# Kernel tuning notes

Hardware: AMD Instinct MI355X
Metric: run time of the kernel (lower is better)

## Reference

```python
import jax, jax.numpy as jnp
import numpy as np

SIZE = 1024
N_ITER = 10
TEMP = 0.125


def setup_inputs() -> dict:
    key = jax.random.key(0)
    k1, k2 = jax.random.split(key)
    x = jax.random.normal(k1, (8, 4096, SIZE), dtype=jnp.float32)
    # weight init: identity + small gaussian noise (matches torch init)
    weight = jnp.eye(SIZE, dtype=jnp.float32) + jax.random.normal(k2, (SIZE, SIZE), dtype=jnp.float32) * 1e-05
    return {"x": x, "weight": weight}


def _sinkhorn_project(weight):
    # log-space Sinkhorn normalization: n_iter steps of symmetric row/col
    # logsumexp subtraction, then exponentiate.
    log_P = weight / TEMP
    for _ in range(N_ITER):
        r_sum = jax.nn.logsumexp(log_P, axis=-1, keepdims=True)  # [size,1]
        c_sum = jax.nn.logsumexp(log_P, axis=-2, keepdims=True)  # [1,size]
        log_P = log_P - 0.5 * (r_sum + c_sum)
    return jnp.exp(log_P)


def reference(x, weight):
    W = _sinkhorn_project(weight)          # [size, size]
    # F.linear(x, W) == x @ W.T
    return jnp.einsum('bsd,od->bso', x, W)
```

## Files before the change

### kernel.cpp

```cpp
#include <hip/hip_runtime.h>
#include <hip/hip_bf16.h>


typedef __attribute__((ext_vector_type(8))) short short8;
typedef __attribute__((ext_vector_type(4))) float f32x4;

__device__ inline unsigned int pk2(float a, float b) {
  __hip_bfloat162 h = __float22bfloat162_rn(make_float2(a, b));
  union { __hip_bfloat162 h; unsigned int u; } cv;
  cv.h = h;
  return cv.u;
}

__global__ void sinkhorn_step(const float* __restrict__ w,
                              const float* __restrict__ Rin,
                              const float* __restrict__ Cin,
                              float* __restrict__ Rout,
                              float* __restrict__ Cout,
                              int first,
                              const float* __restrict__ X,
                              unsigned short* __restrict__ Xb,
                              int do_cvt) {
  __shared__ float4 red4[256];
  const int tid = threadIdx.x;
  const int b = blockIdx.x;
  const int lane = tid & 63, wv = tid >> 6;
  if (b < 256) {
    const int row = 4 * b + wv;
    const float* rp = w + (size_t)row * 1024 + lane * 16;
    float s = 0.f;
    #pragma unroll
    for (int q = 0; q < 4; ++q) {
      float4 v4 = *(const float4*)(rp + q * 4);
      float4 c4 = make_float4(0.f, 0.f, 0.f, 0.f);
      if (!first) c4 = *(const float4*)(Cin + lane * 16 + q * 4);
      s += __expf(8.f * v4.x - 0.5f * c4.x) + __expf(8.f * v4.y - 0.5f * c4.y)
         + __expf(8.f * v4.z - 0.5f * c4.z) + __expf(8.f * v4.w - 0.5f * c4.w);
    }
    #pragma unroll
    for (int off = 32; off > 0; off >>= 1) s += __shfl_down(s, off);
    if (lane == 0)
      Rout[row] = (first ? 0.f : 0.5f * Rin[row]) + __logf(s);
  } else if (b < 320) {
    const int cb = b - 256;
    const int c0 = cb * 16;
    const int rowg = tid >> 2, cg = tid & 3;
    const float* wp = w + (size_t)rowg * 1024 + c0 + cg * 4;
    float ax = 0.f, ay = 0.f, az = 0.f, aw = 0.f;
    #pragma unroll 4
    for (int p = 0; p < 16; ++p) {
      float4 wv4 = *(const float4*)(wp + (size_t)p * 64 * 1024);
      float rp = first ? 0.f : Rin[rowg + p * 64];
      float h = 0.5f * rp;
      ax += __expf(8.f * wv4.x - h);
      ay += __expf(8.f * wv4.y - h);
      az += __expf(8.f * wv4.z - h);
      aw += __expf(8.f * wv4.w - h);
    }
    red4[tid] = make_float4(ax, ay, az, aw);
    __syncthreads();
    if (tid < 16) {
      const int g = tid >> 2, e = tid & 3;
      float s = 0.f;
      #pragma unroll 8
      for (int q = 0; q < 64; ++q)
        s += ((const float*)&red4[q * 4 + g])[e];
      const int col = c0 + tid;
      Cout[col] = (first ? 0.f : 0.5f * Cin[col]) + __logf(s);
    }
  } else if (do_cvt) {
    const size_t idx0 = (size_t)(b - 320) * 256 + tid;
    #pragma unroll
    for (int it = 0; it < 8; ++it) {
      size_t e = (it * 524288ull + idx0) * 8;
      float4 a = *(const float4*)(X + e);
      float4 c = *(const float4*)(X + e + 4);
      uint4 o;
      o.x = pk2(a.x, a.y); o.y = pk2(a.z, a.w);
      o.z = pk2(c.x, c.y); o.w = pk2(c.z, c.w);
      *(uint4*)(Xb + e) = o;
    }
  }
}

__global__ void make_w(const float* __restrict__ w, const float* __restrict__ R,
                       const float* __restrict__ C, unsigned short* __restrict__ Wb) {
  const int i = blockIdx.x;
  const int j = threadIdx.x * 4;
  const float r = 0.5f * R[i];
  float4 v = *(const float4*)(w + (size_t)i * 1024 + j);
  float4 cv = *(const float4*)(C + j);
  unsigned int o[2];
  o[0] = pk2(__expf(8.f * v.x - r - 0.5f * cv.x), __expf(8.f * v.y - r - 0.5f * cv.y));
  o[1] = pk2(__expf(8.f * v.z - r - 0.5f * cv.z), __expf(8.f * v.w - r - 0.5f * cv.w));
  *(uint2*)(Wb + (size_t)i * 1024 + j) = *(uint2*)o;
}

__device__ inline void swizzle_mn(int id, int& m0, int& n0) {
  m0 = ((id & 7) + ((id >> 6) << 3)) << 7;
  n0 = ((id >> 3) & 7) << 7;
}

__global__ __launch_bounds__(256) void gemm_bb(const unsigned short* __restrict__ Xb,
                                               const unsigned short* __restrict__ Wb,
                                               float* __restrict__ out) {
  __shared__ unsigned short As[128 * 64];
  __shared__ unsigned short Bs[128 * 64];
  const int tid = threadIdx.x;
  const int lane = tid & 63, wave = tid >> 6;
  const int wm = wave >> 1, wn = wave & 1;
  int m0, n0;
  swizzle_mn(blockIdx.x, m0, n0);

  f32x4 acc[4][4] = {};
  const int fr = lane & 15, kq = lane >> 4;

  for (int t = 0; t < 16; ++t) {
    const int k0 = t * 64;
    #pragma unroll
    for (int is = 0; is < 4; ++is) {
      int idx = is * 256 + tid;
      int lrow = idx >> 3;
      int g = (idx & 7) ^ (lrow & 7);
      const unsigned short* ga = Xb + (size_t)(m0 + lrow) * 1024 + k0 + g * 8;
      const unsigned short* gb = Wb + (size_t)(n0 + lrow) * 1024 + k0 + g * 8;
      unsigned short* la = As + (size_t)(is * 256 + wave * 64) * 8;
      unsigned short* lb = Bs + (size_t)(is * 256 + wave * 64) * 8;
      __builtin_amdgcn_global_load_lds(
          (const __attribute__((address_space(1))) unsigned int*)ga,
          (__attribute__((address_space(3))) unsigned int*)la, 16, 0, 0);
      __builtin_amdgcn_global_load_lds(
          (const __attribute__((address_space(1))) unsigned int*)gb,
          (__attribute__((address_space(3))) unsigned int*)lb, 16, 0, 0);
    }
    __syncthreads();

    #pragma unroll
    for (int kk = 0; kk < 2; ++kk) {
      short8 af[4], bf[4];
      #pragma unroll
      for (int mt = 0; mt < 4; ++mt) {
        int row = wm * 64 + mt * 16 + fr;
        int cp = (kk * 4 + kq) ^ (row & 7);
        af[mt] = *(const short8*)(As + (size_t)row * 64 + cp * 8);
      }
      #pragma unroll
      for (int nt = 0; nt < 4; ++nt) {
        int row = wn * 64 + nt * 16 + fr;
        int cp = (kk * 4 + kq) ^ (row & 7);
        bf[nt] = *(const short8*)(Bs + (size_t)row * 64 + cp * 8);
      }
      #pragma unroll
      for (int mt = 0; mt < 4; ++mt)
        #pragma unroll
        for (int nt = 0; nt < 4; ++nt)
          acc[mt][nt] = __builtin_amdgcn_mfma_f32_16x16x32_bf16(af[mt], bf[nt], acc[mt][nt], 0, 0, 0);
    }
    __syncthreads();
  }

  const int crow0 = m0 + wm * 64 + (lane >> 4) * 4;
  const int ccol0 = n0 + wn * 64 + fr;
  #pragma unroll
  for (int mt = 0; mt < 4; ++mt)
    #pragma unroll
    for (int nt = 0; nt < 4; ++nt)
      #pragma unroll
      for (int r = 0; r < 4; ++r)
        out[(size_t)(crow0 + mt * 16 + r) * 1024 + ccol0 + nt * 16] = acc[mt][nt][r];
}

__global__ __launch_bounds__(256) void gemm_f(const float* __restrict__ X,
                                              const unsigned short* __restrict__ Wb,
                                              float* __restrict__ out) {
  __shared__ unsigned short As[128 * 64];
  __shared__ unsigned short Bs[128 * 64];
  const int tid = threadIdx.x;
  const int lane = tid & 63, wave = tid >> 6;
  const int wm = wave >> 1, wn = wave & 1;
  int m0, n0;
  swizzle_mn(blockIdx.x, m0, n0);

  f32x4 acc[4][4] = {};
  const int ar = tid >> 1, ah = tid & 1;
  const float* Xrow = X + (size_t)(m0 + ar) * 1024 + ah * 32;
  const int fr = lane & 15, kq = lane >> 4;

  for (int t = 0; t < 16; ++t) {
    const int k0 = t * 64;
    #pragma unroll
    for (int is = 0; is < 4; ++is) {
      int idx = is * 256 + tid;
      int lrow = idx >> 3;
      int g = (idx & 7) ^ (lrow & 7);
      const unsigned short* gb = Wb + (size_t)(n0 + lrow) * 1024 + k0 + g * 8;
      unsigned short* lb = Bs + (size_t)(is * 256 + wave * 64) * 8;
      __builtin_amdgcn_global_load_lds(
          (const __attribute__((address_space(1))) unsigned int*)gb,
          (__attribute__((address_space(3))) unsigned int*)lb, 16, 0, 0);
    }
    #pragma unroll
    for (int q = 0; q < 4; ++q) {
      float4 a = *(const float4*)(Xrow + k0 + q * 8);
      float4 c = *(const float4*)(Xrow + k0 + q * 8 + 4);
      uint4 o;
      o.x = pk2(a.x, a.y); o.y = pk2(a.z, a.w);
      o.z = pk2(c.x, c.y); o.w = pk2(c.z, c.w);
      int cp = (ah * 4 + q) ^ (ar & 7);
      *(uint4*)(As + (size_t)ar * 64 + cp * 8) = o;
    }
    __syncthreads();

    #pragma unroll
    for (int kk = 0; kk < 2; ++kk) {
      short8 af[4], bf[4];
      #pragma unroll
      for (int mt = 0; mt < 4; ++mt) {
        int row = wm * 64 + mt * 16 + fr;
        int cp = (kk * 4 + kq) ^ (row & 7);
        af[mt] = *(const short8*)(As + (size_t)row * 64 + cp * 8);
      }
      #pragma unroll
      for (int nt = 0; nt < 4; ++nt) {
        int row = wn * 64 + nt * 16 + fr;
        int cp = (kk * 4 + kq) ^ (row & 7);
        bf[nt] = *(const short8*)(Bs + (size_t)row * 64 + cp * 8);
      }
      #pragma unroll
      for (int mt = 0; mt < 4; ++mt)
        #pragma unroll
        for (int nt = 0; nt < 4; ++nt)
          acc[mt][nt] = __builtin_amdgcn_mfma_f32_16x16x32_bf16(af[mt], bf[nt], acc[mt][nt], 0, 0, 0);
    }
    __syncthreads();
  }

  const int crow0 = m0 + wm * 64 + (lane >> 4) * 4;
  const int ccol0 = n0 + wn * 64 + fr;
  #pragma unroll
  for (int mt = 0; mt < 4; ++mt)
    #pragma unroll
    for (int nt = 0; nt < 4; ++nt)
      #pragma unroll
      for (int r = 0; r < 4; ++r)
        out[(size_t)(crow0 + mt * 16 + r) * 1024 + ccol0 + nt * 16] = acc[mt][nt][r];
}

__global__ __launch_bounds__(256) void gemm_b(const float* __restrict__ X,
                                              const float* __restrict__ w,
                                              const float* __restrict__ R,
                                              const float* __restrict__ C,
                                              float* __restrict__ out) {
  __shared__ unsigned short As[128 * 32];
  __shared__ unsigned short Bs[128 * 32];
  const int tid = threadIdx.x;
  const int lane = tid & 63, wave = tid >> 6;
  const int wm = wave >> 1, wn = wave & 1;
  int m0, n0;
  swizzle_mn(blockIdx.x, m0, n0);

  f32x4 acc[4][4] = {};
  const int sr = tid >> 1, sk = (tid & 1) * 16;
  const float* Xrow = X + (size_t)(m0 + sr) * 1024 + sk;
  const float* Wrow = w + (size_t)(n0 + sr) * 1024 + sk;
  const float rpot = 0.5f * R[n0 + sr];

  for (int k0 = 0; k0 < 1024; k0 += 32) {
    float4 vb0 = *(const float4*)(Wrow + k0);
    float4 vb1 = *(const float4*)(Wrow + k0 + 4);
    float4 vb2 = *(const float4*)(Wrow + k0 + 8);
    float4 vb3 = *(const float4*)(Wrow + k0 + 12);
    float4 vc0 = *(const float4*)(C + k0 + sk);
    float4 vc1 = *(const float4*)(C + k0 + sk + 4);
    float4 vc2 = *(const float4*)(C + k0 + sk + 8);
    float4 vc3 = *(const float4*)(C + k0 + sk + 12);
    unsigned int pb[8];
    pb[0] = pk2(__expf(8.f * vb0.x - rpot - 0.5f * vc0.x), __expf(8.f * vb0.y - rpot - 0.5f * vc0.y));
    pb[1] = pk2(__expf(8.f * vb0.z - rpot - 0.5f * vc0.z), __expf(8.f * vb0.w - rpot - 0.5f * vc0.w));
    pb[2] = pk2(__expf(8.f * vb1.x - rpot - 0.5f * vc1.x), __expf(8.f * vb1.y - rpot - 0.5f * vc1.y));
    pb[3] = pk2(__expf(8.f * vb1.z - rpot - 0.5f * vc1.z), __expf(8.f * vb1.w - rpot - 0.5f * vc1.w));
    pb[4] = pk2(__expf(8.f * vb2.x - rpot - 0.5f * vc2.x), __expf(8.f * vb2.y - rpot - 0.5f * vc2.y));
    pb[5] = pk2(__expf(8.f * vb2.z - rpot - 0.5f * vc2.z), __expf(8.f * vb2.w - rpot - 0.5f * vc2.w));
    pb[6] = pk2(__expf(8.f * vb3.x - rpot - 0.5f * vc3.x), __expf(8.f * vb3.y - rpot - 0.5f * vc3.y));
    pb[7] = pk2(__expf(8.f * vb3.z - rpot - 0.5f * vc3.z), __expf(8.f * vb3.w - rpot - 0.5f * vc3.w));
    float4 va0 = *(const float4*)(Xrow + k0);
    float4 va1 = *(const float4*)(Xrow + k0 + 4);
    float4 va2 = *(const float4*)(Xrow + k0 + 8);
    float4 va3 = *(const float4*)(Xrow + k0 + 12);
    unsigned int pa[8];
    pa[0] = pk2(va0.x, va0.y); pa[1] = pk2(va0.z, va0.w);
    pa[2] = pk2(va1.x, va1.y); pa[3] = pk2(va1.z, va1.w);
    pa[4] = pk2(va2.x, va2.y); pa[5] = pk2(va2.z, va2.w);
    pa[6] = pk2(va3.x, va3.y); pa[7] = pk2(va3.z, va3.w);

    *(uint4*)(Bs + sr * 32 + sk)     = *(uint4*)(pb);
    *(uint4*)(Bs + sr * 32 + sk + 8) = *(uint4*)(pb + 4);
    *(uint4*)(As + sr * 32 + sk)     = *(uint4*)(pa);
    *(uint4*)(As + sr * 32 + sk + 8) = *(uint4*)(pa + 4);

    __syncthreads();

    const int kq2 = (lane >> 4) * 8;
    const int fr2 = lane & 15;
    short8 af[4], bf[4];
    #pragma unroll
    for (int t = 0; t < 4; ++t)
      af[t] = *(const short8*)(As + (wm * 64 + t * 16 + fr2) * 32 + kq2);
    #pragma unroll
    for (int t = 0; t < 4; ++t)
      bf[t] = *(const short8*)(Bs + (wn * 64 + t * 16 + fr2) * 32 + kq2);
    #pragma unroll
    for (int mt = 0; mt < 4; ++mt)
      #pragma unroll
      for (int nt = 0; nt < 4; ++nt)
        acc[mt][nt] = __builtin_amdgcn_mfma_f32_16x16x32_bf16(af[mt], bf[nt], acc[mt][nt], 0, 0, 0);

    __syncthreads();
  }

  const int crow0 = m0 + wm * 64 + (lane >> 4) * 4;
  const int ccol0 = n0 + wn * 64 + (lane & 15);
  #pragma unroll
  for (int mt = 0; mt < 4; ++mt)
    #pragma unroll
    for (int nt = 0; nt < 4; ++nt)
      #pragma unroll
      for (int r = 0; r < 4; ++r)
        out[(size_t)(crow0 + mt * 16 + r) * 1024 + ccol0 + nt * 16] = acc[mt][nt][r];
}

extern "C" void kernel_launch(void* const* d_in, const int* in_sizes, int n_in,
                              void* d_out, int out_size, void* d_ws, size_t ws_size,
                              hipStream_t stream) {
  const float* x = (const float*)d_in[0];
  const float* weight = (const float*)d_in[1];
  float* out = (float*)d_out;

  float* R0 = (float*)d_ws;
  float* C0 = R0 + 1024;
  float* R1 = C0 + 1024;
  float* C1 = R1 + 1024;
  unsigned short* Wb = (unsigned short*)(C1 + 1024);
  unsigned short* Xb = Wb + (size_t)1024 * 1024;
  const size_t need_small = 16 * 1024 + 2 * 1024 * 1024;
  const size_t need_big = need_small + (size_t)32768 * 1024 * 2;
  const int big = (ws_size >= need_big) ? 1 : 0;
  const int small_ok = (ws_size >= need_small) ? 1 : 0;

  for (int t = 0; t < 10; ++t) {
    const float *Ri, *Ci;
    float *Ro, *Co;
    if ((t & 1) == 0) { Ri = R0; Ci = C0; Ro = R1; Co = C1; }
    else              { Ri = R1; Ci = C1; Ro = R0; Co = C0; }
    const int cvt = (t == 0 && big) ? 1 : 0;
    const int grid = cvt ? 2368 : 320;
    sinkhorn_step<<<grid, 256, 0, stream>>>(weight, Ri, Ci, Ro, Co,
                                            (t == 0) ? 1 : 0, x, Xb, cvt);
  }

  if (small_ok) {
    make_w<<<1024, 256, 0, stream>>>(weight, R0, C0, Wb);
    if (big) gemm_bb<<<2048, 256, 0, stream>>>(Xb, Wb, out);
    else     gemm_f<<<2048, 256, 0, stream>>>(x, Wb, out);
  } else {
    gemm_b<<<2048, 256, 0, stream>>>(x, weight, R0, C0, out);
  }
}
```

Measured before the change: 377.5 us.

## Fuse Sinkhorn iterations into one persistent cooperative kernel with grid barriers

Replaces the ten separate sinkhorn_step launches and the make_w launch with a single cooperative persistent kernel of 256 blocks. Each block keeps its exp(weight/T) row and column slices in registers and runs the iterations in scaling-vector (u,v) form. The blocks synchronise through an atomic counter barrier in workspace, and the x-to-bf16 conversion is spread across the iterations between barrier arrive and wait. This removes per-launch overhead and the repeated weight reads. In exchange it relies on all blocks being co-resident, and a spin limit that can break out before every block arrives, which would give wrong results.

```diff
diff --git a/kernel.cpp b/kernel.cpp
--- a/kernel.cpp
+++ b/kernel.cpp
@@ -10,6 +10,172 @@
   union { __hip_bfloat162 h; unsigned int u; } cv;
   cv.h = h;
   return cv.u;
+}
+
+__device__ __forceinline__ void stc(float* p, float v) {
+  __hip_atomic_store(p, v, __ATOMIC_RELAXED, __HIP_MEMORY_SCOPE_AGENT);
+}
+__device__ __forceinline__ float ldc(const float* p) {
+  return __hip_atomic_load(p, __ATOMIC_RELAXED, __HIP_MEMORY_SCOPE_AGENT);
+}
+
+__global__ __launch_bounds__(256, 1) void sinkhorn_persist(
+    const float* __restrict__ w,
+    int* __restrict__ bar,
+    float* __restrict__ ubuf,
+    float* __restrict__ vbuf,
+    unsigned short* __restrict__ Wb,
+    const float* __restrict__ X,
+    unsigned short* __restrict__ Xb) {
+  __shared__ float uL[1024];
+  __shared__ float vL[1024];
+  __shared__ float redC[4][4];
+  const int k = blockIdx.x;
+  const int t = threadIdx.x;
+  const int l = t & 63, wv = t >> 6;
+  const int row = 4 * k + wv;
+
+  float er[16];
+  {
+    const float* rp = w + (size_t)row * 1024 + l * 16;
+    #pragma unroll
+    for (int q = 0; q < 4; ++q) {
+      float4 v4 = *(const float4*)(rp + q * 4);
+      er[q * 4 + 0] = __expf(8.f * v4.x);
+      er[q * 4 + 1] = __expf(8.f * v4.y);
+      er[q * 4 + 2] = __expf(8.f * v4.z);
+      er[q * 4 + 3] = __expf(8.f * v4.w);
+    }
+  }
+  float ecs[4][4];
+  {
+    #pragma unroll
+    for (int q = 0; q < 4; ++q) {
+      float4 v4 = *(const float4*)(w + (size_t)(4 * t + q) * 1024 + 4 * k);
+      ecs[q][0] = __expf(8.f * v4.x);
+      ecs[q][1] = __expf(8.f * v4.y);
+      ecs[q][2] = __expf(8.f * v4.z);
+      ecs[q][3] = __expf(8.f * v4.w);
+    }
+  }
+
+  float vold = 1.f;
+  float uold = 1.f;
+
+  for (int it = 0; it < 10; ++it) {
+    const int rsl = it & 1;
+    const int wsl = (it + 1) & 1;
+    float ul[16], vvr[4];
+    if (it == 0) {
+      #pragma unroll
+      for (int q = 0; q < 16; ++q) ul[q] = 1.f;
+      vvr[0] = vvr[1] = vvr[2] = vvr[3] = 1.f;
+    } else {
+      {
+        float u0 = ldc(ubuf + rsl * 1024 + t * 4);
+        float u1 = ldc(ubuf + rsl * 1024 + t * 4 + 1);
+        float u2 = ldc(ubuf + rsl * 1024 + t * 4 + 2);
+        float u3 = ldc(ubuf + rsl * 1024 + t * 4 + 3);
+        float v0 = ldc(vbuf + rsl * 1024 + t * 4);
+        float v1 = ldc(vbuf + rsl * 1024 + t * 4 + 1);
+        float v2 = ldc(vbuf + rsl * 1024 + t * 4 + 2);
+        float v3 = ldc(vbuf + rsl * 1024 + t * 4 + 3);
+        int cp = t ^ ((t >> 3) & 7);
+        *(float4*)(uL + cp * 4) = make_float4(u0, u1, u2, u3);
+        *(float4*)(vL + t * 4) = make_float4(v0, v1, v2, v3);
+      }
+      __syncthreads();
+      #pragma unroll
+      for (int q = 0; q < 4; ++q) {
+        int c = l * 4 + q;
+        int cp = c ^ ((c >> 3) & 7);
+        float4 u4 = *(const float4*)(uL + cp * 4);
+        ul[q * 4 + 0] = u4.x; ul[q * 4 + 1] = u4.y;
+        ul[q * 4 + 2] = u4.z; ul[q * 4 + 3] = u4.w;
+      }
+      float4 v4 = *(const float4*)(vL + t * 4);
+      vvr[0] = v4.x; vvr[1] = v4.y; vvr[2] = v4.z; vvr[3] = v4.w;
+    }
+
+    float rs = 0.f;
+    #pragma unroll
+    for (int q = 0; q < 16; ++q) rs += er[q] * ul[q];
+    #pragma unroll
+    for (int off = 32; off > 0; off >>= 1) rs += __shfl_down(rs, off);
+
+    float cs0 = 0.f, cs1 = 0.f, cs2 = 0.f, cs3 = 0.f;
+    #pragma unroll
+    for (int q = 0; q < 4; ++q) {
+      cs0 += ecs[q][0] * vvr[q]; cs1 += ecs[q][1] * vvr[q];
+      cs2 += ecs[q][2] * vvr[q]; cs3 += ecs[q][3] * vvr[q];
+    }
+    #pragma unroll
+    for (int off = 32; off > 0; off >>= 1) {
+      cs0 += __shfl_down(cs0, off); cs1 += __shfl_down(cs1, off);
+      cs2 += __shfl_down(cs2, off); cs3 += __shfl_down(cs3, off);
+    }
+    if (l == 0) {
+      redC[wv][0] = cs0; redC[wv][1] = cs1;
+      redC[wv][2] = cs2; redC[wv][3] = cs3;
+      vold = sqrtf(vold) * rsqrtf(rs);
+      stc(vbuf + wsl * 1024 + row, vold);
+    }
+    __syncthreads();
+    if (wv == 0 && l < 4) {
+      float tot = redC[0][l] + redC[1][l] + redC[2][l] + redC[3][l];
+      uold = sqrtf(uold) * rsqrtf(tot);
+      stc(ubuf + wsl * 1024 + 4 * k + l, uold);
+    }
+
+    asm volatile("s_waitcnt vmcnt(0)" ::: "memory");
+    __syncthreads();
+    if (t == 0)
+      __hip_atomic_fetch_add(bar + it, 1, __ATOMIC_RELAXED, __HIP_MEMORY_SCOPE_AGENT);
+    if (it < 8) {
+      const size_t base = (size_t)k * 131072 + (size_t)it * 16384;
+      #pragma unroll
+      for (int r2 = 0; r2 < 8; ++r2) {
+        size_t e = base + (size_t)(r2 * 256 + t) * 8;
+        float4 a = *(const float4*)(X + e);
+        float4 c = *(const float4*)(X + e + 4);
+        uint4 o;
+        o.x = pk2(a.x, a.y); o.y = pk2(a.z, a.w);
+        o.z = pk2(c.x, c.y); o.w = pk2(c.z, c.w);
+        *(uint4*)(Xb + e) = o;
+      }
+    }
+    if (t == 0) {
+      int spins = 0;
+      while (__hip_atomic_load(bar + it, __ATOMIC_RELAXED, __HIP_MEMORY_SCOPE_AGENT) < 256) {
+        __builtin_amdgcn_s_sleep(2);
+        if (++spins > (1 << 16)) break;
+      }
+    }
+    __syncthreads();
+  }
+
+  {
+    float u0 = ldc(ubuf + t * 4);
+    float u1 = ldc(ubuf + t * 4 + 1);
+    float u2 = ldc(ubuf + t * 4 + 2);
+    float u3 = ldc(ubuf + t * 4 + 3);
+    int cp = t ^ ((t >> 3) & 7);
+    *(float4*)(uL + cp * 4) = make_float4(u0, u1, u2, u3);
+  }
+  __syncthreads();
+  const float vfin = __shfl(vold, 0);
+  unsigned int o[8];
+  #pragma unroll
+  for (int q = 0; q < 4; ++q) {
+    int c = l * 4 + q;
+    int cp = c ^ ((c >> 3) & 7);
+    float4 u4 = *(const float4*)(uL + cp * 4);
+    o[q * 2 + 0] = pk2(er[q * 4 + 0] * vfin * u4.x, er[q * 4 + 1] * vfin * u4.y);
+    o[q * 2 + 1] = pk2(er[q * 4 + 2] * vfin * u4.z, er[q * 4 + 3] * vfin * u4.w);
+  }
+  unsigned short* wp = Wb + (size_t)row * 1024 + l * 16;
+  *(uint4*)(wp) = *(uint4*)(o);
+  *(uint4*)(wp + 8) = *(uint4*)(o + 4);
 }
 
 __global__ void sinkhorn_step(const float* __restrict__ w,
@@ -336,6 +502,40 @@
   const float* weight = (const float*)d_in[1];
   float* out = (float*)d_out;
 
+  int* bar = (int*)d_ws;
+  float* ubufP = (float*)d_ws + 256;
+  float* vbufP = ubufP + 2048;
+  unsigned short* WbP = (unsigned short*)(vbufP + 2048);
+  unsigned short* XbP = WbP + (size_t)1024 * 1024;
+  const size_t need_persist =
+      1024 + 16 * 1024 + 2 * 1024 * 1024 + (size_t)32768 * 1024 * 2;
+
+  if (ws_size >= need_persist) {
+    hipError_t e0 = hipMemsetAsync(bar, 0, 64, stream);
+    if (e0 == hipSuccess) {
+      const float* warg = weight;
+      int* barArg = bar;
+      float* uArg = ubufP;
+      float* vArg = vbufP;
+      unsigned short* WbArg = WbP;
+      const float* xArg = x;
+      unsigned short* XbArg = XbP;
+      void* args[7] = {(void*)&warg, (void*)&barArg, (void*)&uArg,
+                       (void*)&vArg, (void*)&WbArg, (void*)&xArg,
+                       (void*)&XbArg};
+      hipError_t ce = hipLaunchCooperativeKernel((const void*)sinkhorn_persist,
+                                                 dim3(256), dim3(256), args, 0,
+                                                 stream);
+      if (ce == hipSuccess) {
+        gemm_bb<<<2048, 256, 0, stream>>>(XbP, WbP, out);
+        return;
+      }
+      (void)hipGetLastError();
+    } else {
+      (void)hipGetLastError();
+    }
+  }
+
   float* R0 = (float*)d_ws;
   float* C0 = R0 + 1024;
   float* R1 = C0 + 1024;
@@ -357,7 +557,6 @@
     sinkhorn_step<<<grid, 256, 0, stream>>>(weight, Ri, Ci, Ro, Co,
                                             (t == 0) ? 1 : 0, x, Xb, cvt);
   }
-
   if (small_ok) {
     make_w<<<1024, 256, 0, stream>>>(weight, R0, C0, Wb);
     if (big) gemm_bb<<<2048, 256, 0, stream>>>(Xb, Wb, out);
```

Result: slower. 402.9 us (+6.7%).
